# Performance work log

Hardware: AMD Instinct MI355X
Metric: run time of the kernel (lower is better)

## Reference

```python
import jax, jax.numpy as jnp
import numpy as np

B, T, D = 4, 2048, 1024
C_BIAS = 0.0  # init kwarg c
LN_EPS = 1e-5


def setup_inputs() -> dict:
    key = jax.random.key(0)
    ks = jax.random.split(key, 8)
    s = 1.0 / np.sqrt(D)
    return {
        "x": jax.random.normal(ks[0], (B, T, D), dtype=jnp.float32),
        "l": jax.random.randint(ks[1], (B,), 1, T + 1),  # lengths in [1, T]
        "Wq": jax.random.normal(ks[2], (D, D), dtype=jnp.float32) * s,
        "Wk": jax.random.normal(ks[3], (D, D), dtype=jnp.float32) * s,
        "Wv": jax.random.normal(ks[4], (D, D), dtype=jnp.float32) * s,
        "Wo": jax.random.normal(ks[5], (D, D), dtype=jnp.float32) * s,
        "bo": jnp.zeros((D,), dtype=jnp.float32),
        "gamma": jnp.ones((D,), dtype=jnp.float32),
        "beta": jnp.zeros((D,), dtype=jnp.float32),
    }


def reference(x, l, Wq, Wk, Wv, Wo, bo, gamma, beta):
    # LayerNorm over last dim
    mu = jnp.mean(x, axis=-1, keepdims=True)
    var = jnp.mean(jnp.square(x - mu), axis=-1, keepdims=True)
    x_norm = (x - mu) * jax.lax.rsqrt(var + LN_EPS) * gamma + beta

    # QKV projections (torch Linear: y = x @ W.T, no bias)
    q = jnp.einsum("btd,ed->bte", x_norm, Wq)
    k = jnp.einsum("btd,ed->bte", x_norm, Wk)
    v = jnp.einsum("btd,ed->bte", x_norm, Wv)

    scale = 1.0 / jnp.sqrt(jnp.float32(D))
    scores = C_BIAS + jnp.einsum("bid,bjd->bij", q, k) * scale  # [B,T,T]

    # Mask is applied along the ROW (dim 1) axis, and softmax is over dim 1
    # (faithful to the original: mask.unsqueeze(2) + Softmax(dim=1)).
    valid_rows = jnp.arange(T)[None, :] < l[:, None]  # [B,T]
    scores = jnp.where(valid_rows[:, :, None], scores, -jnp.inf)
    attn = jax.nn.softmax(scores, axis=1)  # normalize over rows

    y = x + jnp.einsum("bij,bjd->bid", attn, v)
    out = jax.nn.relu(jnp.einsum("btd,ed->bte", y, Wo) + bo)
    return out
```

## Files before the change

### kernel.cpp

```cpp
#include <hip/hip_runtime.h>
#include <hip/hip_fp16.h>

typedef unsigned short u16;
typedef __attribute__((ext_vector_type(8))) short bf16x8;
typedef __attribute__((ext_vector_type(4))) float f32x4;

#define T_SEQ 2048
#define DIM 1024
#define NB 4
#define NCH 8

__device__ __forceinline__ u16 f2bf(float f) {
  union { float f; unsigned u; } c; c.f = f;
  unsigned r = c.u + 0x7fffu + ((c.u >> 16) & 1u);
  return (u16)(r >> 16);
}

__device__ __forceinline__ void gload_lds16(const void* g, void* l) {
  __builtin_amdgcn_global_load_lds((const __attribute__((address_space(1))) void*)g,
                                   (__attribute__((address_space(3))) void*)l, 16, 0, 0);
}

#define SBAR() asm volatile("s_barrier" ::: "memory")
#define WVL(n) asm volatile("s_waitcnt vmcnt(" n ") lgkmcnt(0)" ::: "memory")

__global__ __launch_bounds__(256) void ln_kernel(const float* __restrict__ x,
                                                 const float* __restrict__ gamma,
                                                 const float* __restrict__ beta,
                                                 u16* __restrict__ xn) {
  const int row = blockIdx.x;
  const int tid = threadIdx.x;
  const float4 v = *(const float4*)(x + (size_t)row * DIM + tid * 4);
  float s  = v.x + v.y + v.z + v.w;
  float ss = v.x * v.x + v.y * v.y + v.z * v.z + v.w * v.w;
#pragma unroll
  for (int o = 32; o > 0; o >>= 1) { s += __shfl_down(s, o); ss += __shfl_down(ss, o); }
  __shared__ float rs[4], rss[4];
  const int wid = tid >> 6, lane = tid & 63;
  if (lane == 0) { rs[wid] = s; rss[wid] = ss; }
  __syncthreads();
  s  = rs[0] + rs[1] + rs[2] + rs[3];
  ss = rss[0] + rss[1] + rss[2] + rss[3];
  const float mu = s * (1.f / DIM);
  const float var = ss * (1.f / DIM) - mu * mu;
  const float rstd = rsqrtf(var + 1e-5f);
  const float4 g  = *(const float4*)(gamma + tid * 4);
  const float4 be = *(const float4*)(beta + tid * 4);
  ushort4 o;
  o.x = f2bf((v.x - mu) * rstd * g.x + be.x);
  o.y = f2bf((v.y - mu) * rstd * g.y + be.y);
  o.z = f2bf((v.z - mu) * rstd * g.z + be.z);
  o.w = f2bf((v.w - mu) * rstd * g.w + be.w);
  *(ushort4*)(xn + (size_t)row * DIM + tid * 4) = o;
}

__global__ __launch_bounds__(256) void wcvt4(const float* __restrict__ wq,
                                             const float* __restrict__ wk,
                                             const float* __restrict__ wv,
                                             const float* __restrict__ wo,
                                             u16* __restrict__ dqk,
                                             u16* __restrict__ dv,
                                             u16* __restrict__ dw) {
  const int sel = blockIdx.x >> 10;
  const size_t t = (size_t)(blockIdx.x & 1023) * 256 + threadIdx.x;
  const float* w = (sel == 0) ? wq : (sel == 1) ? wk : (sel == 2) ? wv : wo;
  u16* d = (sel == 0) ? dqk : (sel == 1) ? (dqk + 1048576) : (sel == 2) ? dv : dw;
  const float4 v = *(const float4*)(w + t * 4);
  ushort4 u; u.x = f2bf(v.x); u.y = f2bf(v.y); u.z = f2bf(v.z); u.w = f2bf(v.w);
  *(ushort4*)(d + t * 4) = u;
}

template <int EPI, int BM>
__global__ __launch_bounds__(512, 2) void gemm_bt(
    const u16* __restrict__ A, const u16* __restrict__ B, void* __restrict__ Cv,
    int K, int lda, int ldb, int ldc,
    long sA, long sB, long sC,
    const float* __restrict__ aux, long sAux, float scale,
    const int* __restrict__ lptr, float* __restrict__ mpQ, float* __restrict__ zpQ) {
  constexpr int MI = BM / 32;
  __shared__ __align__(16) u16 As[4][BM * 32];
  __shared__ __align__(16) u16 Bs[4][256 * 32];
  const int bz = blockIdx.z;
  const u16* Ab = A + (size_t)bz * sA;
  const u16* Bb = B + (size_t)bz * sB;

  const int nb = gridDim.x * gridDim.y;
  int bid = blockIdx.y * gridDim.x + blockIdx.x;
  bid = (bid & 7) * (nb >> 3) + (bid >> 3);
  const int gx = gridDim.x;
  const int tileN = (bid % gx) * 256;
  const int tileM = (bid / gx) * BM;

  const int t = threadIdx.x;
  const int lane = t & 63;
  const int wid = t >> 6;
  const int wm = wid >> 2, wn = wid & 3;

  const int srow = t >> 2;
  const int qsw = (((t & 3) ^ (srow & 3) ^ ((srow >> 2) & 3))) * 8;
  const size_t aoff0 = (size_t)(tileM + srow) * lda + qsw;
  const size_t aoff1 = (size_t)(tileM + 128 + srow) * lda + qsw;
  const size_t boff0 = (size_t)(tileN + srow) * ldb + qsw;
  const size_t boff1 = (size_t)(tileN + 128 + srow) * ldb + qsw;

  const int frow = lane & 15;
  const int kg = lane >> 4;
  const int ckk = ((kg ^ (lane & 3) ^ ((lane >> 2) & 3))) * 8;

  f32x4 acc[MI][4] = {};
  const int NT = K >> 5;

#pragma unroll
  for (int p = 0; p < 3; ++p) {
    const size_t kp = (size_t)p << 5;
    gload_lds16(Ab + aoff0 + kp, &As[p][t * 8]);
    gload_lds16(Bb + boff0 + kp, &Bs[p][t * 8]);
    if constexpr (BM == 256) gload_lds16(Ab + aoff1 + kp, &As[p][4096 + t * 8]);
    gload_lds16(Bb + boff1 + kp, &Bs[p][4096 + t * 8]);
  }
  if constexpr (BM == 256) { asm volatile("s_waitcnt vmcnt(8)" ::: "memory"); }
  else                     { asm volatile("s_waitcnt vmcnt(6)" ::: "memory"); }
  SBAR();

  for (int tau = 0; tau < NT; ++tau) {
    const int cur = tau & 3;
    const int tgt = (tau + 3) & 3;
    const bool st = (tau + 3 < NT);
    const size_t k0 = (size_t)(tau + 3) << 5;

    bf16x8 af[4], bf[4];
#pragma unroll
    for (int j = 0; j < 4; ++j)
      bf[j] = *(const bf16x8*)&Bs[cur][(wn * 64 + j * 16 + frow) * 32 + ckk];
#pragma unroll
    for (int i = 0; i < 4; ++i)
      af[i] = *(const bf16x8*)&As[cur][(wm * (BM / 2) + i * 16 + frow) * 32 + ckk];
    if (st) {
      gload_lds16(Ab + aoff0 + k0, &As[tgt][t * 8]);
      gload_lds16(Bb + boff0 + k0, &Bs[tgt][t * 8]);
      if constexpr (BM == 128) gload_lds16(Bb + boff1 + k0, &Bs[tgt][4096 + t * 8]);
    }
    if constexpr (BM == 128) {
      if (tau < NT - 3) WVL("6"); else if (tau == NT - 3) WVL("3"); else WVL("0");
    }
    SBAR();
    __builtin_amdgcn_s_setprio(1);
#pragma unroll
    for (int i = 0; i < 4; ++i)
#pragma unroll
      for (int j = 0; j < 4; ++j)
        acc[i][j] = __builtin_amdgcn_mfma_f32_16x16x32_bf16(af[i], bf[j], acc[i][j], 0, 0, 0);
    __builtin_amdgcn_s_setprio(0);

    if constexpr (BM == 256) {
      bf16x8 af2[4];
#pragma unroll
      for (int i = 0; i < 4; ++i)
        af2[i] = *(const bf16x8*)&As[cur][(wm * 128 + (4 + i) * 16 + frow) * 32 + ckk];
      if (st) {
        gload_lds16(Ab + aoff1 + k0, &As[tgt][4096 + t * 8]);
        gload_lds16(Bb + boff1 + k0, &Bs[tgt][4096 + t * 8]);
      }
      if (tau < NT - 3) WVL("8"); else if (tau == NT - 3) WVL("4"); else WVL("0");
      SBAR();
      __builtin_amdgcn_s_setprio(1);
#pragma unroll
      for (int i = 0; i < 4; ++i)
#pragma unroll
        for (int j = 0; j < 4; ++j)
          acc[4 + i][j] = __builtin_amdgcn_mfma_f32_16x16x32_bf16(af2[i], bf[j], acc[4 + i][j], 0, 0, 0);
      __builtin_amdgcn_s_setprio(0);
    }
  }

  const int r0 = tileM + wm * (BM / 2) + (kg << 2);
  const int c0 = tileN + wn * 64 + frow;
#pragma unroll
  for (int i = 0; i < MI; ++i)
#pragma unroll
    for (int j = 0; j < 4; ++j)
#pragma unroll
      for (int r = 0; r < 4; ++r) {
        const int row = r0 + i * 16 + r, col = c0 + j * 16;
        const size_t idx = (size_t)row * ldc + col;
        float v = acc[i][j][r];
        if constexpr (EPI == 0) {
          ((u16*)Cv + (size_t)bz * sC)[idx] = f2bf(v);
        } else if constexpr (EPI == 1) {
          ((__half*)Cv + (size_t)bz * sC)[idx] = __float2half(v * scale);
        } else if constexpr (EPI == 2) {
          v += (aux + (size_t)bz * sAux)[idx];
          ((u16*)Cv + (size_t)bz * sC)[idx] = f2bf(v);
        } else {
          v += aux[col];
          ((float*)Cv + (size_t)bz * sC)[idx] = fmaxf(v, 0.f);
        }
      }

  if constexpr (EPI == 1) {
    const int L = lptr[bz];
    __shared__ float2 red[2][4][4][16];
    float Ms[4], Zs[4];
#pragma unroll
    for (int j = 0; j < 4; ++j) {
      float mj = -3e38f;
#pragma unroll
      for (int i = 0; i < MI; ++i)
#pragma unroll
        for (int r = 0; r < 4; ++r) {
          const int row = r0 + i * 16 + r;
          if (row < L) mj = fmaxf(mj, acc[i][j][r] * scale);
        }
      mj = fmaxf(mj, __shfl_xor(mj, 16, 64));
      mj = fmaxf(mj, __shfl_xor(mj, 32, 64));
      float zj = 0.f;
#pragma unroll
      for (int i = 0; i < MI; ++i)
#pragma unroll
        for (int r = 0; r < 4; ++r) {
          const int row = r0 + i * 16 + r;
          if (row < L) zj += __expf(acc[i][j][r] * scale - mj);
        }
      zj += __shfl_xor(zj, 16, 64);
      zj += __shfl_xor(zj, 32, 64);
      Ms[j] = mj; Zs[j] = zj;
    }
    if (lane < 16) {
#pragma unroll
      for (int j = 0; j < 4; ++j) red[wm][wn][j][frow] = make_float2(Ms[j], Zs[j]);
    }
    __syncthreads();
    if (wm == 0 && lane < 16) {
#pragma unroll
      for (int j = 0; j < 4; ++j) {
        const float2 a = red[0][wn][j][frow];
        const float2 b = red[1][wn][j][frow];
        const float M = fmaxf(a.x, b.x);
        const float Z = a.y * __expf(a.x - M) + b.y * __expf(b.x - M);
        const int col = tileN + wn * 64 + j * 16 + frow;
        const size_t o = ((size_t)(tileM >> 8) * NB + bz) * T_SEQ + col;
        mpQ[o] = M; zpQ[o] = Z;
      }
    }
  }
}

__global__ __launch_bounds__(256) void colreduce_comb(const float* __restrict__ mp,
                                                      const float* __restrict__ zp,
                                                      float* __restrict__ m,
                                                      float* __restrict__ rz) {
  const int b = blockIdx.y;
  const int j = blockIdx.x * 256 + threadIdx.x;
  float M = -3e38f, Z = 0.f;
#pragma unroll
  for (int c = 0; c < NCH; ++c) {
    const size_t o = ((size_t)c * NB + b) * T_SEQ + j;
    const float mc = mp[o], zc = zp[o];
    const float nm = fmaxf(M, mc);
    Z = Z * __expf(M - nm) + zc * __expf(mc - nm);
    M = nm;
  }
  m[b * T_SEQ + j] = M;
  rz[b * T_SEQ + j] = 1.f / Z;
}

__global__ __launch_bounds__(256) void pbuild(const __half* __restrict__ S,
                                              const int* __restrict__ l,
                                              const float* __restrict__ m,
                                              const float* __restrict__ rz,
                                              u16* __restrict__ P) {
  const int b = blockIdx.x >> 11;
  const int i = blockIdx.x & (T_SEQ - 1);
  const int j0 = threadIdx.x * 8;
  const size_t off = ((size_t)blockIdx.x << 11) + j0;
  ushort4 o0, o1;
  if (i < l[b]) {
    const __half* sp = S + off;
    const float* mp = m + b * T_SEQ + j0;
    const float* zp = rz + b * T_SEQ + j0;
    u16 tmp[8];
#pragma unroll
    for (int t = 0; t < 8; ++t)
      tmp[t] = f2bf(__expf(__half2float(sp[t]) - mp[t]) * zp[t]);
    o0 = make_ushort4(tmp[0], tmp[1], tmp[2], tmp[3]);
    o1 = make_ushort4(tmp[4], tmp[5], tmp[6], tmp[7]);
  } else {
    o0 = make_ushort4(0, 0, 0, 0);
    o1 = make_ushort4(0, 0, 0, 0);
  }
  *(ushort4*)(P + off) = o0;
  *(ushort4*)(P + off + 4) = o1;
}

extern "C" void kernel_launch(void* const* d_in, const int* in_sizes, int n_in,
                              void* d_out, int out_size, void* d_ws, size_t ws_size,
                              hipStream_t stream) {
  (void)in_sizes; (void)n_in; (void)out_size; (void)ws_size;
  const float* x     = (const float*)d_in[0];
  const int*   l     = (const int*)d_in[1];
  const float* Wq    = (const float*)d_in[2];
  const float* Wk    = (const float*)d_in[3];
  const float* Wv    = (const float*)d_in[4];
  const float* Wo    = (const float*)d_in[5];
  const float* bo    = (const float*)d_in[6];
  const float* gamma = (const float*)d_in[7];
  const float* beta  = (const float*)d_in[8];

  char* ws = (char*)d_ws;
  const size_t MiB = 1024 * 1024;
  u16* xn   = (u16*)(ws);
  u16* wqkb = (u16*)(ws + 16 * MiB);
  u16* wvb  = (u16*)(ws + 20 * MiB);
  u16* wob  = (u16*)(ws + 22 * MiB);
  u16* QKb  = (u16*)(ws + 24 * MiB);
  u16* Vt   = (u16*)(ws + 56 * MiB);
  float* mpart = (float*)(ws + 20 * MiB);
  float* zpart = (float*)(ws + 20 * MiB + 512 * 1024);
  float* mb  = (float*)(ws + 72 * MiB);
  float* rzb = (float*)(ws + 72 * MiB + 32 * 1024);
  u16* Pb = QKb;
  u16* yb = xn;
  __half* S = (__half*)d_out;
  float* outp = (float*)d_out;

  const long TD = (long)T_SEQ * DIM, TT = (long)T_SEQ * T_SEQ;
  const long TQK = (long)T_SEQ * 2048;

  ln_kernel<<<NB * T_SEQ, 256, 0, stream>>>(x, gamma, beta, xn);
  wcvt4<<<4096, 256, 0, stream>>>(Wq, Wk, Wv, Wo, wqkb, wvb, wob);

  gemm_bt<0, 256><<<dim3(8, 32, 1), 512, 0, stream>>>(
      xn, wqkb, QKb, DIM, DIM, DIM, 2048, 0, 0, 0, nullptr, 0, 0.f,
      nullptr, nullptr, nullptr);
  gemm_bt<0, 128><<<dim3(32, 8, 1), 512, 0, stream>>>(
      wvb, xn, Vt, DIM, DIM, DIM, 8192, 0, 0, 0, nullptr, 0, 0.f,
      nullptr, nullptr, nullptr);
  gemm_bt<1, 256><<<dim3(8, 8, NB), 512, 0, stream>>>(
      QKb, QKb + 1024, S, DIM, 2048, 2048, T_SEQ, TQK, TQK, TT, nullptr, 0, 0.03125f,
      l, mpart, zpart);
  colreduce_comb<<<dim3(T_SEQ / 256, NB), 256, 0, stream>>>(mpart, zpart, mb, rzb);
  pbuild<<<NB * T_SEQ, 256, 0, stream>>>(S, l, mb, rzb, Pb);
  gemm_bt<2, 128><<<dim3(4, 16, NB), 512, 0, stream>>>(
      Pb, Vt, yb, T_SEQ, T_SEQ, 8192, DIM, TT, 2048, TD, x, TD, 0.f,
      nullptr, nullptr, nullptr);
  gemm_bt<3, 128><<<dim3(4, 64, 1), 512, 0, stream>>>(
      yb, wob, outp, DIM, DIM, DIM, DIM, 0, 0, 0, bo, 0, 0.f,
      nullptr, nullptr, nullptr);
}
```

Measured before the change: 210.0 us.

## Skip masked rows across QK projection, score GEMM, colreduce and P build

Uses the per-batch valid length l to skip tile work for rows that are masked. The Q projection tiles beyond l return early, score GEMM tiles with tileM >= l exit, and colreduce only combines chunks that hold valid rows. pbuild skips rows past l rounded up to 128, and the PV GEMM writes y = x directly for fully masked row tiles. This removes GEMM and elementwise work that scales with T when l is short, at the cost of early-exit branches and leaving some buffers unwritten. Correctness depends on later stages never reading those buffers.

```diff
diff --git a/kernel.cpp b/kernel.cpp
--- a/kernel.cpp
+++ b/kernel.cpp
@@ -70,7 +70,7 @@
   *(ushort4*)(d + t * 4) = u;
 }
 
-template <int EPI, int BM>
+template <int EPI, int BM, int MSK>
 __global__ __launch_bounds__(512, 2) void gemm_bt(
     const u16* __restrict__ A, const u16* __restrict__ B, void* __restrict__ Cv,
     int K, int lda, int ldb, int ldc,
@@ -92,6 +92,31 @@
   const int tileM = (bid / gx) * BM;
 
   const int t = threadIdx.x;
+
+  if constexpr (MSK == 1) {
+    if (tileM >= lptr[bz]) return;
+  }
+  if constexpr (MSK == 3) {
+    if (((tileM & (T_SEQ - 1)) >= lptr[tileM >> 11]) && tileN < DIM) return;
+  }
+  if constexpr (MSK == 2) {
+    if (tileM >= lptr[bz]) {
+      const float* xb = aux + (size_t)bz * sAux;
+      u16* yo = (u16*)Cv + (size_t)bz * sC;
+      for (int e = t; e < (BM * 256) / 8; e += 512) {
+        const int row = tileM + (e >> 5);
+        const int col = tileN + ((e & 31) << 3);
+        const float4 v0 = *(const float4*)(xb + (size_t)row * ldc + col);
+        const float4 v1 = *(const float4*)(xb + (size_t)row * ldc + col + 4);
+        ushort4 o0; o0.x = f2bf(v0.x); o0.y = f2bf(v0.y); o0.z = f2bf(v0.z); o0.w = f2bf(v0.w);
+        ushort4 o1; o1.x = f2bf(v1.x); o1.y = f2bf(v1.y); o1.z = f2bf(v1.z); o1.w = f2bf(v1.w);
+        *(ushort4*)(yo + (size_t)row * ldc + col) = o0;
+        *(ushort4*)(yo + (size_t)row * ldc + col + 4) = o1;
+      }
+      return;
+    }
+  }
+
   const int lane = t & 63;
   const int wid = t >> 6;
   const int wm = wid >> 2, wn = wid & 3;
@@ -247,13 +272,14 @@
 
 __global__ __launch_bounds__(256) void colreduce_comb(const float* __restrict__ mp,
                                                       const float* __restrict__ zp,
+                                                      const int* __restrict__ l,
                                                       float* __restrict__ m,
                                                       float* __restrict__ rz) {
   const int b = blockIdx.y;
   const int j = blockIdx.x * 256 + threadIdx.x;
+  const int L = l[b];
   float M = -3e38f, Z = 0.f;
-#pragma unroll
-  for (int c = 0; c < NCH; ++c) {
+  for (int c = 0; c < NCH && (c << 8) < L; ++c) {
     const size_t o = ((size_t)c * NB + b) * T_SEQ + j;
     const float mc = mp[o], zc = zp[o];
     const float nm = fmaxf(M, mc);
@@ -271,10 +297,12 @@
                                               u16* __restrict__ P) {
   const int b = blockIdx.x >> 11;
   const int i = blockIdx.x & (T_SEQ - 1);
+  const int L = l[b];
+  if (i >= ((L + 127) & ~127)) return;
   const int j0 = threadIdx.x * 8;
   const size_t off = ((size_t)blockIdx.x << 11) + j0;
   ushort4 o0, o1;
-  if (i < l[b]) {
+  if (i < L) {
     const __half* sp = S + off;
     const float* mp = m + b * T_SEQ + j0;
     const float* zp = rz + b * T_SEQ + j0;
@@ -329,21 +357,21 @@
   ln_kernel<<<NB * T_SEQ, 256, 0, stream>>>(x, gamma, beta, xn);
   wcvt4<<<4096, 256, 0, stream>>>(Wq, Wk, Wv, Wo, wqkb, wvb, wob);
 
-  gemm_bt<0, 256><<<dim3(8, 32, 1), 512, 0, stream>>>(
+  gemm_bt<0, 256, 3><<<dim3(8, 32, 1), 512, 0, stream>>>(
       xn, wqkb, QKb, DIM, DIM, DIM, 2048, 0, 0, 0, nullptr, 0, 0.f,
-      nullptr, nullptr, nullptr);
-  gemm_bt<0, 128><<<dim3(32, 8, 1), 512, 0, stream>>>(
+      l, nullptr, nullptr);
+  gemm_bt<0, 128, 0><<<dim3(32, 8, 1), 512, 0, stream>>>(
       wvb, xn, Vt, DIM, DIM, DIM, 8192, 0, 0, 0, nullptr, 0, 0.f,
       nullptr, nullptr, nullptr);
-  gemm_bt<1, 256><<<dim3(8, 8, NB), 512, 0, stream>>>(
+  gemm_bt<1, 256, 1><<<dim3(8, 8, NB), 512, 0, stream>>>(
       QKb, QKb + 1024, S, DIM, 2048, 2048, T_SEQ, TQK, TQK, TT, nullptr, 0, 0.03125f,
       l, mpart, zpart);
-  colreduce_comb<<<dim3(T_SEQ / 256, NB), 256, 0, stream>>>(mpart, zpart, mb, rzb);
+  colreduce_comb<<<dim3(T_SEQ / 256, NB), 256, 0, stream>>>(mpart, zpart, l, mb, rzb);
   pbuild<<<NB * T_SEQ, 256, 0, stream>>>(S, l, mb, rzb, Pb);
-  gemm_bt<2, 128><<<dim3(4, 16, NB), 512, 0, stream>>>(
+  gemm_bt<2, 128, 2><<<dim3(4, 16, NB), 512, 0, stream>>>(
       Pb, Vt, yb, T_SEQ, T_SEQ, 8192, DIM, TT, 2048, TD, x, TD, 0.f,
-      nullptr, nullptr, nullptr);
-  gemm_bt<3, 128><<<dim3(4, 64, 1), 512, 0, stream>>>(
+      l, nullptr, nullptr);
+  gemm_bt<3, 128, 0><<<dim3(4, 64, 1), 512, 0, stream>>>(
       yb, wob, outp, DIM, DIM, DIM, DIM, 0, 0, 0, bo, 0, 0.f,
       nullptr, nullptr, nullptr);
 }
```

Result: no change. 208.4 us (-0.8%).
